# Kernel optimization log

Hardware: AMD Instinct MI355X
Metric: run time of the kernel (lower is better)

Reference implementation:

```python
import jax, jax.numpy as jnp
import numpy as np

# AdaptiveSoftmax.forward (fairseq), no adaptive_inputs, dropout=0 (eval-equivalent).
# cutoff after __init__ appends vocab_size: [10000, 30000, 50000]
CUTOFF = (10000, 30000, 50000)


def setup_inputs() -> dict:
    key = jax.random.key(0)
    ks = jax.random.split(key, 7)
    B, T, D = 2, 2048, 1024
    head_dim = CUTOFF[0] + (len(CUTOFF) - 1)  # 10002
    d0 = int(D // 4.0 ** 1)  # 256
    d1 = int(D // 4.0 ** 2)  # 64
    inp = {
        "input": jax.random.normal(ks[0], (B, T, D), jnp.float32),
        "target": jax.random.randint(ks[1], (B, T), 0, CUTOFF[-1], jnp.int32),
        # xavier-ish scaled params
        "head_w": jax.random.normal(ks[2], (head_dim, D), jnp.float32) * 0.02,
        "proj0_w": jax.random.normal(ks[3], (d0, D), jnp.float32) * 0.04,
        "out0_w": jax.random.normal(ks[4], (CUTOFF[1] - CUTOFF[0], d0), jnp.float32) * 0.02,
        "proj1_w": jax.random.normal(ks[5], (d1, D), jnp.float32) * 0.06,
        "out1_w": jax.random.normal(ks[6], (CUTOFF[2] - CUTOFF[1], d1), jnp.float32) * 0.02,
    }
    return inp


def reference(input, target, head_w, proj0_w, out0_w, proj1_w, out1_w):
    c0, c1, c2 = CUTOFF
    D = input.shape[-1]
    h = input.reshape(-1, D)            # [N, D] (dropout p=0 -> identity)
    t = target.reshape(-1)              # [N]

    # band membership masks (adapt_target routing)
    m0 = (t >= c0) & (t < c1)
    m1 = (t >= c1) & (t < c2)

    # new_target[0]: tail tokens remapped to class slots c0+i
    new_t_head = jnp.where(m0, c0, jnp.where(m1, c0 + 1, t))
    # per-band relative targets (0 for rows not in the band; original returns
    # ragged gathered targets -- here dense+masked equivalent)
    new_t0 = jnp.where(m0, t - c0, 0)
    new_t1 = jnp.where(m1, t - c1, 0)

    # head: Linear(D -> c0 + n_tails, bias=False)
    head_out = jnp.einsum('nd,vd->nv', h, head_w)  # [N, 10002]

    # tails: proj (D->dim) then out (dim->band_size); original applies only to
    # gathered band rows -- dense version masked to zero outside the band
    # computes the same values on band rows.
    tail0 = jnp.einsum('nk,vk->nv', jnp.einsum('nd,kd->nk', h, proj0_w), out0_w)
    tail0 = tail0 * m0[:, None].astype(tail0.dtype)  # [N, 20000]
    tail1 = jnp.einsum('nk,vk->nv', jnp.einsum('nd,kd->nk', h, proj1_w), out1_w)
    tail1 = tail1 * m1[:, None].astype(tail1.dtype)  # [N, 20000]

    return (head_out, tail0, tail1, new_t_head, new_t0, new_t1)
```

## Files before the change

### kernel.cpp

```cpp
#include <hip/hip_runtime.h>

#define C0 10000
#define C1 30000
#define C2 50000

typedef __attribute__((ext_vector_type(8))) short short8;
typedef __attribute__((ext_vector_type(8))) unsigned short ushort8;
typedef __attribute__((ext_vector_type(4))) float f32x4;

__device__ __forceinline__ unsigned short f2bf(float f) {
    unsigned int u = __float_as_uint(f);
    u += 0x7FFF + ((u >> 16) & 1);
    return (unsigned short)(u >> 16);
}

#define SZ_IN    (4096 * 1024)
#define OFF_IN   0
#define HW_ROWSP 10240
#define SZ_HW    (HW_ROWSP * 1024)
#define REAL_HW  (10002 * 1024)
#define OFF_HW   (OFF_IN + SZ_IN)
#define OFF_PJ   (OFF_HW + SZ_HW)
#define SZ_PJ    (512 * 1024)
#define PJ_P0    (256 * 1024)
#define PJ_P1    (64 * 1024)
#define O_ROWSP  20224
#define SZ_O0    (O_ROWSP * 256)
#define REAL_O0  (20000 * 256)
#define OFF_O0   (OFF_PJ + SZ_PJ)
#define SZ_O1    (O_ROWSP * 64)
#define REAL_O1  (20000 * 64)
#define OFF_O1   (OFF_O0 + SZ_O0)
#define CVT_TOTAL (OFF_O1 + SZ_O1)
#define OFF_PP0C CVT_TOTAL
#define SZ_PP0C  (4096 * 256)
#define OFF_PP1C (OFF_PP0C + SZ_PP0C)
#define SZ_PP1C  (4096 * 64)
#define OFF_IDX  (OFF_PP1C + SZ_PP1C)

__global__ __launch_bounds__(256) void convert_kernel(
    const float* __restrict__ in,  const float* __restrict__ hw,
    const float* __restrict__ p0w, const float* __restrict__ o0w,
    const float* __restrict__ p1w, const float* __restrict__ o1w,
    unsigned short* __restrict__ ws,
    const int* __restrict__ target,
    float* __restrict__ o3, float* __restrict__ o4, float* __restrict__ o5)
{
    long long tid = (long long)blockIdx.x * blockDim.x + threadIdx.x;
    if (tid < 4096) {
        int tg = target[tid];
        bool m0 = (tg >= C0) && (tg < C1);
        bool m1 = (tg >= C1) && (tg < C2);
        o3[tid] = (float)(m0 ? C0 : (m1 ? (C0 + 1) : tg));
        o4[tid] = (float)(m0 ? (tg - C0) : 0);
        o5[tid] = (float)(m1 ? (tg - C1) : 0);
    }
    long long i = tid * 8;
    if (i >= CVT_TOTAL) return;
    const float* src;
    long long rel, real;
    if (i < OFF_HW)                      { src = in;  rel = i - OFF_IN;            real = SZ_IN;   }
    else if (i < OFF_PJ)                 { src = hw;  rel = i - OFF_HW;            real = REAL_HW; }
    else if (i < OFF_PJ + PJ_P0)         { src = p0w; rel = i - OFF_PJ;            real = PJ_P0;   }
    else if (i < OFF_PJ + PJ_P0 + PJ_P1) { src = p1w; rel = i - (OFF_PJ + PJ_P0);  real = PJ_P1;   }
    else if (i < OFF_O0)                 { src = p1w; rel = 1;                     real = 0;       }
    else if (i < OFF_O1)                 { src = o0w; rel = i - OFF_O0;            real = REAL_O0; }
    else                                 { src = o1w; rel = i - OFF_O1;            real = REAL_O1; }
    ushort8 o;
    if (rel < real) {
        float4 v0 = *(const float4*)(src + rel);
        float4 v1 = *(const float4*)(src + rel + 4);
        o[0] = f2bf(v0.x); o[1] = f2bf(v0.y); o[2] = f2bf(v0.z); o[3] = f2bf(v0.w);
        o[4] = f2bf(v1.x); o[5] = f2bf(v1.y); o[6] = f2bf(v1.z); o[7] = f2bf(v1.w);
    } else {
        o = (ushort8)0;
    }
    *(ushort8*)(ws + i) = o;
}

__global__ __launch_bounds__(1024) void build_idx(const int* __restrict__ target,
                                                  int* __restrict__ idx0,
                                                  int* __restrict__ idx1,
                                                  int* __restrict__ cnts)
{
    __shared__ int wsum0[16], wsum1[16];
    __shared__ int base0, base1;
    const int t = threadIdx.x, lane = t & 63, wv = t >> 6;
    if (t == 0) { base0 = 0; base1 = 0; }
    __syncthreads();
    for (int r = 0; r < 4; r++) {
        int i = r * 1024 + t;
        int tg = target[i];
        bool p0 = (tg >= C0) && (tg < C1);
        bool p1 = (tg >= C1) && (tg < C2);
        unsigned long long b0 = __ballot(p0);
        unsigned long long b1 = __ballot(p1);
        int pre0 = __popcll(b0 & ((1ull << lane) - 1));
        int pre1 = __popcll(b1 & ((1ull << lane) - 1));
        if (lane == 0) { wsum0[wv] = __popcll(b0); wsum1[wv] = __popcll(b1); }
        __syncthreads();
        int woff0 = base0, woff1 = base1;
        for (int k = 0; k < wv; k++) { woff0 += wsum0[k]; woff1 += wsum1[k]; }
        if (p0) idx0[woff0 + pre0] = i;
        if (p1) idx1[woff1 + pre1] = i;
        __syncthreads();
        if (t == 0) {
            for (int k = 0; k < 16; k++) { base0 += wsum0[k]; base1 += wsum1[k]; }
        }
        __syncthreads();
    }
    for (int j = base0 + t; j < 4096; j += 1024) idx0[j] = 0;
    for (int j = base1 + t; j < 4096; j += 1024) idx1[j] = 0;
    if (t == 0) { cnts[0] = base0; cnts[1] = base1; }
}

#define BM 128
#define BN 128
#define BK 64

__global__ __launch_bounds__(256) void proj_gather(
    const unsigned short* __restrict__ A,
    const unsigned short* __restrict__ pjw,
    unsigned short* __restrict__ pp0c, unsigned short* __restrict__ pp1c,
    const int* __restrict__ idx0, const int* __restrict__ idx1,
    const int* __restrict__ cnts)
{
    const int band = blockIdx.z;
    if (band == 1 && blockIdx.x > 0) return;
    const int* idx = band ? idx1 : idx0;
    const int cnt = cnts[band];
    const int mBase = blockIdx.y * BM;
    if (mBase >= cnt) return;
    const unsigned short* B = pjw + (band ? (size_t)PJ_P0 : 0);
    const int Nn = band ? 64 : 256;
    unsigned short* Cb = band ? pp1c : pp0c;
    const int K = 1024;

    __shared__ unsigned short As[BM * BK];
    __shared__ unsigned short Bs[BN * BK];

    const int t    = threadIdx.x;
    const int lane = t & 63;
    const int w    = t >> 6;
    const int wr   = w >> 1;
    const int wc   = w & 1;
    const int nBase = blockIdx.x * BN;
    const int srow = lane >> 3;
    const int scol = (lane & 7) * 8;

    int rowsIdx[4];
    #pragma unroll
    for (int c = 0; c < 4; c++)
        rowsIdx[c] = idx[mBase + w * 32 + c * 8 + srow];

    f32x4 acc[4][4] = {};

    for (int k0 = 0; k0 < K; k0 += BK) {
        #pragma unroll
        for (int c = 0; c < 4; c++) {
            const int rbase = w * 32 + c * 8;
            const unsigned short* ga = A + (size_t)rowsIdx[c] * K + k0 + scol;
            __builtin_amdgcn_global_load_lds(
                (const __attribute__((address_space(1))) void*)ga,
                (__attribute__((address_space(3))) void*)&As[rbase * BK], 16, 0, 0);
            const unsigned short* gb = B + (size_t)(nBase + rbase + srow) * K + k0 + scol;
            __builtin_amdgcn_global_load_lds(
                (const __attribute__((address_space(1))) void*)gb,
                (__attribute__((address_space(3))) void*)&Bs[rbase * BK], 16, 0, 0);
        }
        __syncthreads();

        #pragma unroll
        for (int kk = 0; kk < BK / 32; kk++) {
            const int kOff = kk * 32 + (lane >> 4) * 8;
            short8 a4[4], b4[4];
            #pragma unroll
            for (int m = 0; m < 4; m++)
                a4[m] = *(const short8*)(&As[(wr * 64 + m * 16 + (lane & 15)) * BK + kOff]);
            #pragma unroll
            for (int n = 0; n < 4; n++)
                b4[n] = *(const short8*)(&Bs[(wc * 64 + n * 16 + (lane & 15)) * BK + kOff]);
            #pragma unroll
            for (int m = 0; m < 4; m++)
                #pragma unroll
                for (int n = 0; n < 4; n++)
                    acc[m][n] = __builtin_amdgcn_mfma_f32_16x16x32_bf16(
                        a4[m], b4[n], acc[m][n], 0, 0, 0);
        }
        __syncthreads();
    }

    #pragma unroll
    for (int m = 0; m < 4; m++)
        #pragma unroll
        for (int i = 0; i < 4; i++) {
            int grow = mBase + wr * 64 + m * 16 + (lane >> 4) * 4 + i;
            #pragma unroll
            for (int n = 0; n < 4; n++) {
                int gcol = nBase + wc * 64 + n * 16 + (lane & 15);
                if (gcol < Nn)
                    Cb[(size_t)grow * Nn + gcol] = f2bf(acc[m][n][i]);
            }
        }
}


__device__ __forceinline__ short8 ldsw(const unsigned short* base, int row, int chunk) {
    int slot = chunk ^ (row & 7);
    return *(const short8*)(base + row * 64 + slot * 8);
}

#define STG(dstElemOff, srcPtr)                                                \
  __builtin_amdgcn_global_load_lds(                                            \
      (const __attribute__((address_space(1))) void*)(srcPtr),                 \
      (__attribute__((address_space(3))) void*)(lds + (dstElemOff)), 16, 0, 0);

#define STAGE_A(bf, h, kofs) {                                                 \
    STG((bf)*32768 + (h)*8192 + (w * 8) * 64,        pA[h] + (kofs));          \
    STG((bf)*32768 + (h)*8192 + (64 + w * 8) * 64,   pA[h] + (size_t)64 * K + (kofs)); }
#define STAGE_B(bf, h, kofs) {                                                 \
    STG((bf)*32768 + 16384 + (h)*8192 + (w * 8) * 64,      pB[h] + (kofs));    \
    STG((bf)*32768 + 16384 + (h)*8192 + (64 + w * 8) * 64, pB[h] + (size_t)64 * K + (kofs)); }

#define VM4()  asm volatile("s_waitcnt vmcnt(4)" ::: "memory")
#define BARF() { __builtin_amdgcn_s_barrier(); asm volatile("" ::: "memory"); }

#define NB_FUSED 3200
#define TAIL_SLOTS 2528

__global__ __launch_bounds__(512) void fused_kernel(
    const unsigned short* __restrict__ in_bf, const unsigned short* __restrict__ hw_bf,
    const unsigned short* __restrict__ pp0c,  const unsigned short* __restrict__ pp1c,
    const unsigned short* __restrict__ o0w,   const unsigned short* __restrict__ o1w,
    float* __restrict__ head_out, float* __restrict__ tail0, float* __restrict__ tail1,
    const int* __restrict__ idx0, const int* __restrict__ idx1,
    const int* __restrict__ cnts, const int* __restrict__ target)
{
    __shared__ unsigned short lds[65536];

    const int L    = blockIdx.x;
    const int t    = threadIdx.x;
    const int lane = t & 63;
    const int w    = t >> 6;
    const int wm   = w >> 2;
    const int wn   = w & 3;
    const int lr   = lane & 15;
    const int lq   = lane >> 4;
    const int lr3  = lane >> 3;
    const int swzc = ((lane & 7) ^ lr3) * 8;

    const unsigned short *A = nullptr, *B = nullptr;
    float* Cp = nullptr;
    const int* idx = nullptr;
    int K = 0, NT = 0, Nn = 0, Mlimit = 0, mBase = 0, nBase = 0;
    bool live = false;

    if (L % 5 == 0) {
        int h = L / 5;
        int swz = (h & 7) * 80 + (h >> 3);
        nBase = (swz >> 4) * 256;
        mBase = (swz & 15) * 256;
        A = in_bf; B = hw_bf; Cp = head_out;
        K = 1024; NT = 16; Nn = 10002; Mlimit = 4096;
        live = true;
    } else {
        int s = L - L / 5 - 1;
        if (s < TAIL_SLOTS) {
            int band = s / 1264;
            int r    = s % 1264;
            nBase = (r / 16) * 256;
            mBase = (r % 16) * 256;
            if (band == 0) { A = pp0c; B = o0w; Cp = tail0; idx = idx0; K = 256; NT = 4; }
            else           { A = pp1c; B = o1w; Cp = tail1; idx = idx1; K = 64;  NT = 1; }
            Nn = 20000;
            Mlimit = cnts[band];
            live = (mBase < Mlimit);
        }
    }

    if (live) {
        const unsigned short* pA[2];
        const unsigned short* pB[2];
        #pragma unroll
        for (int h = 0; h < 2; h++) {
            pA[h] = A + (size_t)(mBase + h * 128 + w * 8 + lr3) * K + swzc;
            pB[h] = B + (size_t)(nBase + h * 128 + w * 8 + lr3) * K + swzc;
        }

        f32x4 acc[8][4] = {};
        short8 af[4][2], bf0[2][2], bf1[2][2];

        STAGE_A(0, 0, 0); STAGE_B(0, 0, 0); STAGE_B(0, 1, 0); STAGE_A(0, 1, 0);

        for (int kt = 0; kt < NT; ++kt) {
            const int cb = kt & 1, nb2 = cb ^ 1;
            const int kofs = (kt + 1) * 64;
            const unsigned short* Ab0 = lds + cb * 32768;
            const unsigned short* Ab1 = Ab0 + 8192;
            const unsigned short* Bb0 = Ab0 + 16384;
            const unsigned short* Bb1 = Ab0 + 24576;

            VM4(); BARF();
            #pragma unroll
            for (int m = 0; m < 4; m++)
                #pragma unroll
                for (int ks = 0; ks < 2; ks++)
                    af[m][ks] = ldsw(Ab0, wm * 64 + m * 16 + lr, ks * 4 + lq);
            #pragma unroll
            for (int n = 0; n < 2; n++)
                #pragma unroll
                for (int ks = 0; ks < 2; ks++)
                    bf0[n][ks] = ldsw(Bb0, wn * 32 + n * 16 + lr, ks * 4 + lq);
            STAGE_A(nb2, 0, kofs);
            __builtin_amdgcn_s_setprio(1);
            #pragma unroll
            for (int m = 0; m < 4; m++)
                #pragma unroll
                for (int n = 0; n < 2; n++)
                    #pragma unroll
                    for (int ks = 0; ks < 2; ks++)
                        acc[m][n] = __builtin_amdgcn_mfma_f32_16x16x32_bf16(
                            af[m][ks], bf0[n][ks], acc[m][n], 0, 0, 0);
            __builtin_amdgcn_s_setprio(0);

            VM4(); BARF();
            #pragma unroll
            for (int n = 0; n < 2; n++)
                #pragma unroll
                for (int ks = 0; ks < 2; ks++)
                    bf1[n][ks] = ldsw(Bb1, wn * 32 + n * 16 + lr, ks * 4 + lq);
            STAGE_B(nb2, 0, kofs);
            __builtin_amdgcn_s_setprio(1);
            #pragma unroll
            for (int m = 0; m < 4; m++)
                #pragma unroll
                for (int n = 0; n < 2; n++)
                    #pragma unroll
                    for (int ks = 0; ks < 2; ks++)
                        acc[m][2 + n] = __builtin_amdgcn_mfma_f32_16x16x32_bf16(
                            af[m][ks], bf1[n][ks], acc[m][2 + n], 0, 0, 0);
            __builtin_amdgcn_s_setprio(0);

            VM4(); BARF();
            #pragma unroll
            for (int m = 0; m < 4; m++)
                #pragma unroll
                for (int ks = 0; ks < 2; ks++)
                    af[m][ks] = ldsw(Ab1, wm * 64 + m * 16 + lr, ks * 4 + lq);
            STAGE_B(nb2, 1, kofs);
            __builtin_amdgcn_s_setprio(1);
            #pragma unroll
            for (int m = 0; m < 4; m++)
                #pragma unroll
                for (int n = 0; n < 2; n++)
                    #pragma unroll
                    for (int ks = 0; ks < 2; ks++)
                        acc[4 + m][2 + n] = __builtin_amdgcn_mfma_f32_16x16x32_bf16(
                            af[m][ks], bf1[n][ks], acc[4 + m][2 + n], 0, 0, 0);
            __builtin_amdgcn_s_setprio(0);

            BARF();
            STAGE_A(nb2, 1, kofs);
            __builtin_amdgcn_s_setprio(1);
            #pragma unroll
            for (int m = 0; m < 4; m++)
                #pragma unroll
                for (int n = 0; n < 2; n++)
                    #pragma unroll
                    for (int ks = 0; ks < 2; ks++)
                        acc[4 + m][n] = __builtin_amdgcn_mfma_f32_16x16x32_bf16(
                            af[m][ks], bf0[n][ks], acc[4 + m][n], 0, 0, 0);
            __builtin_amdgcn_s_setprio(0);
        }

        #pragma unroll
        for (int m = 0; m < 8; m++) {
            const int growb = mBase + (m >> 2) * 128 + wm * 64 + (m & 3) * 16 + lq * 4;
            #pragma unroll
            for (int i = 0; i < 4; i++) {
                int grow = growb + i;
                if (grow < Mlimit) {
                    int gr = idx ? idx[grow] : grow;
                    #pragma unroll
                    for (int n = 0; n < 4; n++) {
                        int gcol = nBase + (n >> 1) * 128 + wn * 32 + (n & 1) * 16 + lr;
                        if (gcol < Nn)
                            Cp[(size_t)gr * Nn + gcol] = acc[m][n][i];
                    }
                }
            }
        }
    }

    for (int j = L; j < 8192; j += NB_FUSED) {
        int row   = j >> 1;
        int which = j & 1;
        int tg = target[row];
        bool in = which ? (tg >= C1 && tg < C2) : (tg >= C0 && tg < C1);
        if (!in) {
            float4* dst = (float4*)((which ? tail1 : tail0) + (size_t)row * 20000);
            float4 z = {0.f, 0.f, 0.f, 0.f};
            for (int q = t; q < 5000; q += 512) dst[q] = z;
        }
    }
}

extern "C" void kernel_launch(void* const* d_in, const int* in_sizes, int n_in,
                              void* d_out, int out_size, void* d_ws, size_t ws_size,
                              hipStream_t stream)
{
    const float* input   = (const float*)d_in[0];
    const int*   target  = (const int*)  d_in[1];
    const float* head_w  = (const float*)d_in[2];
    const float* proj0_w = (const float*)d_in[3];
    const float* out0_w  = (const float*)d_in[4];
    const float* proj1_w = (const float*)d_in[5];
    const float* out1_w  = (const float*)d_in[6];

    const int N = 4096;

    float* out      = (float*)d_out;
    float* head_out = out;
    float* tail0    = head_out + (size_t)N * 10002;
    float* tail1    = tail0 + (size_t)N * 20000;
    float* o3       = tail1 + (size_t)N * 20000;
    float* o4       = o3 + N;
    float* o5       = o4 + N;

    unsigned short* ws = (unsigned short*)d_ws;
    unsigned short* in_bf  = ws + OFF_IN;
    unsigned short* hw_bf  = ws + OFF_HW;
    unsigned short* pjw_bf = ws + OFF_PJ;
    unsigned short* o0w_bf = ws + OFF_O0;
    unsigned short* o1w_bf = ws + OFF_O1;
    unsigned short* pp0c   = ws + OFF_PP0C;
    unsigned short* pp1c   = ws + OFF_PP1C;
    int* idx0 = (int*)(ws + OFF_IDX);
    int* idx1 = idx0 + 4096;
    int* cnts = idx1 + 4096;

    convert_kernel<<<dim3((CVT_TOTAL / 8 + 255) / 256), dim3(256), 0, stream>>>(
        input, head_w, proj0_w, out0_w, proj1_w, out1_w, ws, target, o3, o4, o5);

    build_idx<<<dim3(1), dim3(1024), 0, stream>>>(target, idx0, idx1, cnts);

    proj_gather<<<dim3(2, N / BM, 2), dim3(256), 0, stream>>>(
        in_bf, pjw_bf, pp0c, pp1c, idx0, idx1, cnts);

    fused_kernel<<<dim3(NB_FUSED), dim3(512), 0, stream>>>(
        in_bf, hw_bf, pp0c, pp1c, o0w_bf, o1w_bf,
        head_out, tail0, tail1, idx0, idx1, cnts, target);
}
```

Baseline: 322.4 us.

## Restructure GEMM main loop into batched staging plus four barrier-fenced MFMA phases

The fused GEMM loop now issues all global-to-LDS loads for the next k-tile at the top of each iteration with a single vmcnt wait, instead of spreading the staging across the four compute sub-phases. Each wave now owns a contiguous 128x64 output block instead of interleaved halves, which changes the LDS fragment addressing and the epilogue index math. Each of the four MFMA phases is fenced by two barriers and a full lgkmcnt wait. The aim is simpler, more regular overlap of memory and compute, but the extra barriers and full LDS waits may reduce overlap between LDS reads and MFMA issue.

New measurement: 355.1 us. 1.1x slower.

```diff
diff --git a/kernel.cpp b/kernel.cpp
--- a/kernel.cpp
+++ b/kernel.cpp
@@ -210,20 +210,43 @@
     return *(const short8*)(base + row * 64 + slot * 8);
 }
 
+#define PHASE(MO, NO, LOADA)                                                   \
+  {                                                                            \
+    if (LOADA) {                                                               \
+      _Pragma("unroll") for (int m = 0; m < 4; m++)                            \
+        _Pragma("unroll") for (int ks = 0; ks < 2; ks++)                       \
+          af[m][ks] = ldsw(Ab, (MO + m) * 16 + lr, ks * 4 + lq);               \
+    }                                                                          \
+    _Pragma("unroll") for (int n = 0; n < 2; n++)                              \
+      _Pragma("unroll") for (int ks = 0; ks < 2; ks++)                         \
+        bfrag[n][ks] = ldsw(Bb, brow0 + (NO + n) * 16 + lr, ks * 4 + lq);      \
+    __builtin_amdgcn_s_barrier();                                              \
+    asm volatile("s_waitcnt lgkmcnt(0)" ::: "memory");                         \
+    __builtin_amdgcn_s_setprio(1);                                             \
+    _Pragma("unroll") for (int m = 0; m < 4; m++)                              \
+      _Pragma("unroll") for (int n = 0; n < 2; n++)                            \
+        _Pragma("unroll") for (int ks = 0; ks < 2; ks++)                       \
+          acc[MO + m][NO + n] = __builtin_amdgcn_mfma_f32_16x16x32_bf16(       \
+              af[m][ks], bfrag[n][ks], acc[MO + m][NO + n], 0, 0, 0);          \
+    __builtin_amdgcn_s_setprio(0);                                             \
+    __builtin_amdgcn_s_barrier();                                              \
+  }
+
 #define STG(dstElemOff, srcPtr)                                                \
   __builtin_amdgcn_global_load_lds(                                            \
       (const __attribute__((address_space(1))) void*)(srcPtr),                 \
       (__attribute__((address_space(3))) void*)(lds + (dstElemOff)), 16, 0, 0);
 
-#define STAGE_A(bf, h, kofs) {                                                 \
-    STG((bf)*32768 + (h)*8192 + (w * 8) * 64,        pA[h] + (kofs));          \
-    STG((bf)*32768 + (h)*8192 + (64 + w * 8) * 64,   pA[h] + (size_t)64 * K + (kofs)); }
-#define STAGE_B(bf, h, kofs) {                                                 \
-    STG((bf)*32768 + 16384 + (h)*8192 + (w * 8) * 64,      pB[h] + (kofs));    \
-    STG((bf)*32768 + 16384 + (h)*8192 + (64 + w * 8) * 64, pB[h] + (size_t)64 * K + (kofs)); }
-
-#define VM4()  asm volatile("s_waitcnt vmcnt(4)" ::: "memory")
-#define BARF() { __builtin_amdgcn_s_barrier(); asm volatile("" ::: "memory"); }
+#define STAGE(bufi, kofs)                                                      \
+  {                                                                            \
+    _Pragma("unroll") for (int hh = 0; hh < 2; hh++)                           \
+      _Pragma("unroll") for (int cc = 0; cc < 2; cc++) {                       \
+        STG((bufi) * 32768 + hh * 8192 + (cc * 64 + w * 8) * 64,               \
+            srcA[hh][cc] + (kofs));                                            \
+        STG((bufi) * 32768 + 16384 + hh * 8192 + (cc * 64 + w * 8) * 64,       \
+            srcB[hh][cc] + (kofs));                                            \
+      }                                                                        \
+  }
 
 #define NB_FUSED 3200
 #define TAIL_SLOTS 2528
@@ -248,6 +271,7 @@
     const int lq   = lane >> 4;
     const int lr3  = lane >> 3;
     const int swzc = ((lane & 7) ^ lr3) * 8;
+    const int brow0 = (wn & 1) * 64;
 
     const unsigned short *A = nullptr, *B = nullptr;
     float* Cp = nullptr;
@@ -279,103 +303,37 @@
     }
 
     if (live) {
-        const unsigned short* pA[2];
-        const unsigned short* pB[2];
+        const unsigned short* srcA[2][2];
+        const unsigned short* srcB[2][2];
         #pragma unroll
-        for (int h = 0; h < 2; h++) {
-            pA[h] = A + (size_t)(mBase + h * 128 + w * 8 + lr3) * K + swzc;
-            pB[h] = B + (size_t)(nBase + h * 128 + w * 8 + lr3) * K + swzc;
-        }
+        for (int hh = 0; hh < 2; hh++)
+            #pragma unroll
+            for (int cc = 0; cc < 2; cc++) {
+                int rrow = hh * 128 + cc * 64 + w * 8 + lr3;
+                srcA[hh][cc] = A + (size_t)(mBase + rrow) * K + swzc;
+                srcB[hh][cc] = B + (size_t)(nBase + rrow) * K + swzc;
+            }
 
         f32x4 acc[8][4] = {};
-        short8 af[4][2], bf0[2][2], bf1[2][2];
-
-        STAGE_A(0, 0, 0); STAGE_B(0, 0, 0); STAGE_B(0, 1, 0); STAGE_A(0, 1, 0);
-
+        short8 af[4][2], bfrag[2][2];
+
+        STAGE(0, 0);
         for (int kt = 0; kt < NT; ++kt) {
-            const int cb = kt & 1, nb2 = cb ^ 1;
-            const int kofs = (kt + 1) * 64;
-            const unsigned short* Ab0 = lds + cb * 32768;
-            const unsigned short* Ab1 = Ab0 + 8192;
-            const unsigned short* Bb0 = Ab0 + 16384;
-            const unsigned short* Bb1 = Ab0 + 24576;
-
-            VM4(); BARF();
-            #pragma unroll
-            for (int m = 0; m < 4; m++)
-                #pragma unroll
-                for (int ks = 0; ks < 2; ks++)
-                    af[m][ks] = ldsw(Ab0, wm * 64 + m * 16 + lr, ks * 4 + lq);
-            #pragma unroll
-            for (int n = 0; n < 2; n++)
-                #pragma unroll
-                for (int ks = 0; ks < 2; ks++)
-                    bf0[n][ks] = ldsw(Bb0, wn * 32 + n * 16 + lr, ks * 4 + lq);
-            STAGE_A(nb2, 0, kofs);
-            __builtin_amdgcn_s_setprio(1);
-            #pragma unroll
-            for (int m = 0; m < 4; m++)
-                #pragma unroll
-                for (int n = 0; n < 2; n++)
-                    #pragma unroll
-                    for (int ks = 0; ks < 2; ks++)
-                        acc[m][n] = __builtin_amdgcn_mfma_f32_16x16x32_bf16(
-                            af[m][ks], bf0[n][ks], acc[m][n], 0, 0, 0);
-            __builtin_amdgcn_s_setprio(0);
-
-            VM4(); BARF();
-            #pragma unroll
-            for (int n = 0; n < 2; n++)
-                #pragma unroll
-                for (int ks = 0; ks < 2; ks++)
-                    bf1[n][ks] = ldsw(Bb1, wn * 32 + n * 16 + lr, ks * 4 + lq);
-            STAGE_B(nb2, 0, kofs);
-            __builtin_amdgcn_s_setprio(1);
-            #pragma unroll
-            for (int m = 0; m < 4; m++)
-                #pragma unroll
-                for (int n = 0; n < 2; n++)
-                    #pragma unroll
-                    for (int ks = 0; ks < 2; ks++)
-                        acc[m][2 + n] = __builtin_amdgcn_mfma_f32_16x16x32_bf16(
-                            af[m][ks], bf1[n][ks], acc[m][2 + n], 0, 0, 0);
-            __builtin_amdgcn_s_setprio(0);
-
-            VM4(); BARF();
-            #pragma unroll
-            for (int m = 0; m < 4; m++)
-                #pragma unroll
-                for (int ks = 0; ks < 2; ks++)
-                    af[m][ks] = ldsw(Ab1, wm * 64 + m * 16 + lr, ks * 4 + lq);
-            STAGE_B(nb2, 1, kofs);
-            __builtin_amdgcn_s_setprio(1);
-            #pragma unroll
-            for (int m = 0; m < 4; m++)
-                #pragma unroll
-                for (int n = 0; n < 2; n++)
-                    #pragma unroll
-                    for (int ks = 0; ks < 2; ks++)
-                        acc[4 + m][2 + n] = __builtin_amdgcn_mfma_f32_16x16x32_bf16(
-                            af[m][ks], bf1[n][ks], acc[4 + m][2 + n], 0, 0, 0);
-            __builtin_amdgcn_s_setprio(0);
-
-            BARF();
-            STAGE_A(nb2, 1, kofs);
-            __builtin_amdgcn_s_setprio(1);
-            #pragma unroll
-            for (int m = 0; m < 4; m++)
-                #pragma unroll
-                for (int n = 0; n < 2; n++)
-                    #pragma unroll
-                    for (int ks = 0; ks < 2; ks++)
-                        acc[4 + m][n] = __builtin_amdgcn_mfma_f32_16x16x32_bf16(
-                            af[m][ks], bf0[n][ks], acc[4 + m][n], 0, 0, 0);
-            __builtin_amdgcn_s_setprio(0);
+            const int buf = kt & 1;
+            STAGE(buf ^ 1, (kt + 1) * 64);
+            asm volatile("s_waitcnt vmcnt(8)" ::: "memory");
+            __builtin_amdgcn_s_barrier();
+            const unsigned short* Ab = lds + buf * 32768 + wm * 8192;
+            const unsigned short* Bb = lds + buf * 32768 + 16384 + (wn >> 1) * 8192;
+            PHASE(0, 0, 1)
+            PHASE(0, 2, 0)
+            PHASE(4, 0, 1)
+            PHASE(4, 2, 0)
         }
 
         #pragma unroll
         for (int m = 0; m < 8; m++) {
-            const int growb = mBase + (m >> 2) * 128 + wm * 64 + (m & 3) * 16 + lq * 4;
+            const int growb = mBase + wm * 128 + m * 16 + lq * 4;
             #pragma unroll
             for (int i = 0; i < 4; i++) {
                 int grow = growb + i;
@@ -383,7 +341,7 @@
                     int gr = idx ? idx[grow] : grow;
                     #pragma unroll
                     for (int n = 0; n < 4; n++) {
-                        int gcol = nBase + (n >> 1) * 128 + wn * 32 + (n & 1) * 16 + lr;
+                        int gcol = nBase + wn * 64 + n * 16 + lr;
                         if (gcol < Nn)
                             Cp[(size_t)gr * Nn + gcol] = acc[m][n][i];
                     }
```
